# Optimization experiments

Measured on AMD Instinct MI355X. Metric: run time of the kernel, lower is better.

The kernel has to match this reference:

```python
import jax, jax.numpy as jnp
import numpy as np

NUM_CLASSES = 4
STRENGTH_INTER = 1.0
MOMENTUM = 0.99
EPS = 1e-8
LOG2 = 0.6931471805599453


def setup_inputs() -> dict:
    key = jax.random.key(0)
    k1, k2, k3, k4 = jax.random.split(key, 4)
    B, F, C, D, H, W = 2, 32, NUM_CLASSES, 64, 128, 128
    return {
        "features_to_modulate": jax.random.normal(k1, (B, F, D, H, W), dtype=jnp.float32),
        "logits_A": jax.random.normal(k2, (B, C, D, H, W), dtype=jnp.float32),
        "logits_B": jax.random.normal(k3, (B, C, D, H, W), dtype=jnp.float32),
        "pseudo_labels": jax.random.randint(k4, (B, D, H, W), 0, C, dtype=jnp.int64),
        "global_class_ranks": jnp.arange(C, dtype=jnp.float32),
    }


def _gamma_map(logits_A, logits_B, pseudo_labels, global_class_ranks):
    # JS-divergence disagreement map, summed over class channel (axis=1)
    logpA = jax.nn.log_softmax(logits_A, axis=1)
    logpB = jax.nn.log_softmax(logits_B, axis=1)
    pA = jnp.exp(logpA)
    pB = jnp.exp(logpB)
    logM = jnp.log(0.5 * (pA + pB) + EPS)
    kl_A = jnp.sum(pA * (logpA - logM), axis=1)  # [B,D,H,W]
    kl_B = jnp.sum(pB * (logpB - logM), axis=1)
    dis = 0.5 * (kl_A + kl_B)

    # per-class stats via segment reductions (single pass instead of per-class masking)
    lab_flat = pseudo_labels.reshape(-1)
    dis_flat = dis.reshape(-1)
    counts = jax.ops.segment_sum(jnp.ones_like(dis_flat), lab_flat, num_segments=NUM_CLASSES)
    seg_min = jax.ops.segment_min(dis_flat, lab_flat, num_segments=NUM_CLASSES)
    seg_max = jax.ops.segment_max(dis_flat, lab_flat, num_segments=NUM_CLASSES)
    present = counts > 0
    # EMA buffers start uninitialized (init: min=0, max=log 2); first call copies batch stats
    cls_min = jnp.where(present, seg_min, 0.0)
    cls_max = jnp.where(present, seg_max, LOG2)

    dmin = cls_min[pseudo_labels]
    dmax = cls_max[pseudo_labels]
    norm = jnp.where(dmax > dmin, (dis - dmin) / (dmax - dmin + EPS), 0.5)

    inter_term = 1.0 - global_class_ranks / (NUM_CLASSES - 1)
    inter_map = STRENGTH_INTER * inter_term[pseudo_labels]
    return 1.0 + inter_map * norm  # [B,D,H,W]


def reference(features_to_modulate, logits_A, logits_B, pseudo_labels, global_class_ranks):
    gamma_map = _gamma_map(logits_A, logits_B, pseudo_labels, global_class_ranks)
    scaled = features_to_modulate * gamma_map[:, None]  # broadcast over channel dim
    return scaled, gamma_map
```

## Files before the change

### kernel.cpp

```cpp
#include <hip/hip_runtime.h>
#include <hip/hip_bf16.h>

#define S_VOX  1048576
#define NVOX   2097152
#define NCLS   4
#define NFEAT  32
#define FEAT_ELEMS 67108864
#define EPS_F  1e-8f
#define LOG2_F 0.6931471805599453f
#define DIS_BLOCKS 1024

typedef float f32x4 __attribute__((ext_vector_type(4)));

__device__ __forceinline__ unsigned f2key(float f) {
    unsigned u = __float_as_uint(f);
    return (u & 0x80000000u) ? ~u : (u | 0x80000000u);
}
__device__ __forceinline__ float key2f(unsigned k) {
    unsigned u = (k & 0x80000000u) ? (k & 0x7FFFFFFFu) : ~k;
    return __uint_as_float(u);
}


__global__ void k_prolog(const unsigned* __restrict__ lab32, int* __restrict__ flag) {
    int t = threadIdx.x;
    unsigned even = lab32[2 * t];
    unsigned odd  = lab32[2 * t + 1];
    unsigned long long oddnz  = __ballot(odd  != 0u);
    unsigned long long evennz = __ballot(even != 0u);
    if (t == 0) *flag = (oddnz == 0ull && evennz != 0ull) ? 1 : 0;
}

__global__ void __launch_bounds__(256)
k_dis(const float* __restrict__ lA, const float* __restrict__ lB,
      const unsigned* __restrict__ lab32, const int* __restrict__ i64flag,
      float* __restrict__ dis, unsigned* __restrict__ partials) {
    __shared__ unsigned smin[NCLS], smax[NCLS];
    if (threadIdx.x < NCLS) { smin[threadIdx.x] = 0xFFFFFFFFu; smax[threadIdx.x] = 0u; }
    __syncthreads();

    const int lstride = 1 + *i64flag;
    unsigned lmin[NCLS] = {0xFFFFFFFFu, 0xFFFFFFFFu, 0xFFFFFFFFu, 0xFFFFFFFFu};
    unsigned lmax[NCLS] = {0u, 0u, 0u, 0u};

    const int nquad = NVOX / 4;
    for (int q = blockIdx.x * blockDim.x + threadIdx.x; q < nquad;
         q += gridDim.x * blockDim.x) {
        const int g = q << 2;
        const int b = g >> 20;
        const int v = g & (S_VOX - 1);
        const size_t abase = ((size_t)b * NCLS) * S_VOX + v;

        float4 a0 = *(const float4*)(lA + abase);
        float4 a1 = *(const float4*)(lA + abase + S_VOX);
        float4 a2 = *(const float4*)(lA + abase + 2 * (size_t)S_VOX);
        float4 a3 = *(const float4*)(lA + abase + 3 * (size_t)S_VOX);
        float4 c0 = *(const float4*)(lB + abase);
        float4 c1 = *(const float4*)(lB + abase + S_VOX);
        float4 c2 = *(const float4*)(lB + abase + 2 * (size_t)S_VOX);
        float4 c3 = *(const float4*)(lB + abase + 3 * (size_t)S_VOX);

        float dv[4];
        #pragma unroll
        for (int j = 0; j < 4; ++j) {
            float av[NCLS] = { ((const float*)&a0)[j], ((const float*)&a1)[j],
                               ((const float*)&a2)[j], ((const float*)&a3)[j] };
            float bv[NCLS] = { ((const float*)&c0)[j], ((const float*)&c1)[j],
                               ((const float*)&c2)[j], ((const float*)&c3)[j] };
            float maxA = fmaxf(fmaxf(av[0], av[1]), fmaxf(av[2], av[3]));
            float maxB = fmaxf(fmaxf(bv[0], bv[1]), fmaxf(bv[2], bv[3]));
            float eA[NCLS], eB[NCLS];
            float sA = 0.f, sB = 0.f;
            #pragma unroll
            for (int c = 0; c < NCLS; ++c) {
                eA[c] = __expf(av[c] - maxA); sA += eA[c];
                eB[c] = __expf(bv[c] - maxB); sB += eB[c];
            }
            float lseA = __logf(sA), lseB = __logf(sB);
            float rsA = 1.f / sA, rsB = 1.f / sB;
            float kl = 0.f;
            #pragma unroll
            for (int c = 0; c < NCLS; ++c) {
                float pA  = eA[c] * rsA;
                float pB  = eB[c] * rsB;
                float la  = av[c] - maxA - lseA;
                float lb  = bv[c] - maxB - lseB;
                float lM  = __logf(0.5f * (pA + pB) + EPS_F);
                kl += pA * (la - lM) + pB * (lb - lM);
            }
            dv[j] = 0.5f * kl;
        }

        *(float4*)(dis + g) = make_float4(dv[0], dv[1], dv[2], dv[3]);

        #pragma unroll
        for (int j = 0; j < 4; ++j) {
            int lbl = (int)lab32[(size_t)(g + j) * lstride];
            unsigned key = f2key(dv[j]);
            #pragma unroll
            for (int c = 0; c < NCLS; ++c) {
                if (lbl == c) {
                    lmin[c] = min(lmin[c], key);
                    lmax[c] = max(lmax[c], key);
                }
            }
        }
    }

    #pragma unroll
    for (int off = 32; off > 0; off >>= 1) {
        #pragma unroll
        for (int c = 0; c < NCLS; ++c) {
            unsigned om = (unsigned)__shfl_xor((int)lmin[c], off);
            unsigned oM = (unsigned)__shfl_xor((int)lmax[c], off);
            lmin[c] = min(lmin[c], om);
            lmax[c] = max(lmax[c], oM);
        }
    }
    if ((threadIdx.x & 63) == 0) {
        #pragma unroll
        for (int c = 0; c < NCLS; ++c) {
            atomicMin(&smin[c], lmin[c]);
            atomicMax(&smax[c], lmax[c]);
        }
    }
    __syncthreads();
    if (threadIdx.x < 8) {
        unsigned val = (threadIdx.x < NCLS) ? smin[threadIdx.x] : smax[threadIdx.x - NCLS];
        partials[(size_t)blockIdx.x * 8 + threadIdx.x] = val;
    }
}

__global__ void __launch_bounds__(256)
k_stats(const unsigned* __restrict__ partials, const float* __restrict__ ranks,
        float* __restrict__ params) {
    __shared__ unsigned red[4][8];
    const int tid = threadIdx.x;

    unsigned mn[NCLS] = {0xFFFFFFFFu, 0xFFFFFFFFu, 0xFFFFFFFFu, 0xFFFFFFFFu};
    unsigned mx[NCLS] = {0u, 0u, 0u, 0u};
    #pragma unroll
    for (int s = 0; s < 4; ++s) {
        const unsigned* p = partials + ((size_t)tid * 4 + s) * 8;
        uint4 pmin = *(const uint4*)(p);
        uint4 pmax = *(const uint4*)(p + 4);
        mn[0] = min(mn[0], pmin.x); mn[1] = min(mn[1], pmin.y);
        mn[2] = min(mn[2], pmin.z); mn[3] = min(mn[3], pmin.w);
        mx[0] = max(mx[0], pmax.x); mx[1] = max(mx[1], pmax.y);
        mx[2] = max(mx[2], pmax.z); mx[3] = max(mx[3], pmax.w);
    }
    #pragma unroll
    for (int off = 32; off > 0; off >>= 1) {
        #pragma unroll
        for (int c = 0; c < NCLS; ++c) {
            unsigned om = (unsigned)__shfl_xor((int)mn[c], off);
            unsigned oM = (unsigned)__shfl_xor((int)mx[c], off);
            mn[c] = min(mn[c], om);
            mx[c] = max(mx[c], oM);
        }
    }
    if ((tid & 63) == 0) {
        const int w = tid >> 6;
        #pragma unroll
        for (int c = 0; c < NCLS; ++c) { red[w][c] = mn[c]; red[w][NCLS + c] = mx[c]; }
    }
    __syncthreads();
    if (tid < NCLS) {
        const int c = tid;
        unsigned kmin = 0xFFFFFFFFu, kmax = 0u;
        #pragma unroll
        for (int w = 0; w < 4; ++w) {
            kmin = min(kmin, red[w][c]);
            kmax = max(kmax, red[w][NCLS + c]);
        }
        bool present = (kmin != 0xFFFFFFFFu);
        float dmin = present ? key2f(kmin) : 0.0f;
        float dmax = present ? key2f(kmax) : LOG2_F;
        float inter = 1.0f - ranks[c] * (1.0f / (NCLS - 1));
        float base, mult;
        if (dmax > dmin) {
            float inv = 1.0f / (dmax - dmin + EPS_F);
            mult = inter * inv;
            base = 1.0f - mult * dmin;
        } else {
            mult = 0.0f;
            base = 1.0f + 0.5f * inter;
        }
        params[c] = base;
        params[NCLS + c] = mult;
    }
}

__global__ void __launch_bounds__(256)
k_gamma(const unsigned* __restrict__ lab32, const int* __restrict__ i64flag,
        const float* __restrict__ dis, const float* __restrict__ params,
        float* __restrict__ gamma_out) {
    const int q = blockIdx.x * blockDim.x + threadIdx.x;
    const int g = q << 2;
    if (g >= NVOX) return;
    const int lstride = 1 + *i64flag;

    float4 d4 = *(const float4*)(dis + g);
    float ga[4];
    #pragma unroll
    for (int j = 0; j < 4; ++j) {
        int lbl = (int)lab32[(size_t)(g + j) * lstride];
        ga[j] = params[lbl] + params[NCLS + lbl] * ((const float*)&d4)[j];
    }
    *(float4*)(gamma_out + g) = make_float4(ga[0], ga[1], ga[2], ga[3]);
}

__global__ void __launch_bounds__(256)
k_scale(const float* __restrict__ feat, const float* __restrict__ gamma,
        float* __restrict__ out) {
    const size_t nchunk = FEAT_ELEMS / 4 / 512;
    for (size_t cb = blockIdx.x; cb < nchunk; cb += gridDim.x) {
        const size_t q0 = cb * 512 + threadIdx.x;
        const size_t e0 = q0 << 2;
        const size_t e1 = e0 + 1024;
        const size_t g0 = ((e0 >> 25) << 20) + (e0 & (size_t)(S_VOX - 1));
        const size_t g1 = ((e1 >> 25) << 20) + (e1 & (size_t)(S_VOX - 1));
        f32x4 x0 = __builtin_nontemporal_load((const f32x4*)(feat + e0));
        f32x4 x1 = __builtin_nontemporal_load((const f32x4*)(feat + e1));
        f32x4 m0 = *(const f32x4*)(gamma + g0);
        f32x4 m1 = *(const f32x4*)(gamma + g1);
        __builtin_nontemporal_store(x0 * m0, (f32x4*)(out + e0));
        __builtin_nontemporal_store(x1 * m1, (f32x4*)(out + e1));
    }
}

extern "C" void kernel_launch(void* const* d_in, const int* in_sizes, int n_in,
                              void* d_out, int out_size, void* d_ws, size_t ws_size,
                              hipStream_t stream) {
    const float*    feat  = (const float*)d_in[0];
    const float*    lA    = (const float*)d_in[1];
    const float*    lB    = (const float*)d_in[2];
    const unsigned* lab32 = (const unsigned*)d_in[3];
    const float*    ranks = (const float*)d_in[4];
    float* out = (float*)d_out;

    char* ws = (char*)d_ws;
    int*      flag     = (int*)(ws + 32);
    float*    params   = (float*)(ws + 64);
    float*    dis      = (float*)(ws + 256);
    unsigned* partials = (unsigned*)(ws + 256 + (size_t)NVOX * 4);

    float* gamma_out = out + (size_t)FEAT_ELEMS;

    k_prolog<<<1, 64, 0, stream>>>(lab32, flag);
    k_dis<<<DIS_BLOCKS, 256, 0, stream>>>(lA, lB, lab32, flag, dis, partials);
    k_stats<<<1, 256, 0, stream>>>(partials, ranks, params);
    k_gamma<<<NVOX / 4 / 256, 256, 0, stream>>>(lab32, flag, dis, params, gamma_out);
    k_scale<<<8192, 256, 0, stream>>>(feat, gamma_out, out);
}
```

Baseline: 130.7 us.

## Fuse gamma computation into scale kernel using label-packed dis values

Packs the 2-bit pseudo label into the low mantissa bits of each disagreement value, so one 32-bit word carries both. The separate gamma kernel is removed: the scale kernel rebuilds gamma from the packed word and the per-class params, multiplies the features, and the feature-0 blocks also write the gamma output. This drops one launch and the extra read and write pass over dis, labels and gamma. In exchange the two low mantissa bits of dis are dropped (a small precision loss), and gamma is recomputed once for each of the 32 feature channels.

```diff
diff --git a/kernel.cpp b/kernel.cpp
--- a/kernel.cpp
+++ b/kernel.cpp
@@ -34,7 +34,7 @@
 __global__ void __launch_bounds__(256)
 k_dis(const float* __restrict__ lA, const float* __restrict__ lB,
       const unsigned* __restrict__ lab32, const int* __restrict__ i64flag,
-      float* __restrict__ dis, unsigned* __restrict__ partials) {
+      unsigned* __restrict__ disp, unsigned* __restrict__ partials) {
     __shared__ unsigned smin[NCLS], smax[NCLS];
     if (threadIdx.x < NCLS) { smin[threadIdx.x] = 0xFFFFFFFFu; smax[threadIdx.x] = 0u; }
     __syncthreads();
@@ -91,15 +91,23 @@
             dv[j] = 0.5f * kl;
         }
 
-        *(float4*)(dis + g) = make_float4(dv[0], dv[1], dv[2], dv[3]);
+        unsigned lbls[4];
+        #pragma unroll
+        for (int j = 0; j < 4; ++j)
+            lbls[j] = lab32[(size_t)(g + j) * lstride] & 3u;
+
+        unsigned pw[4];
+        #pragma unroll
+        for (int j = 0; j < 4; ++j)
+            pw[j] = (__float_as_uint(dv[j]) & ~3u) | lbls[j];
+        *(uint4*)(disp + g) = make_uint4(pw[0], pw[1], pw[2], pw[3]);
 
         #pragma unroll
         for (int j = 0; j < 4; ++j) {
-            int lbl = (int)lab32[(size_t)(g + j) * lstride];
             unsigned key = f2key(dv[j]);
             #pragma unroll
             for (int c = 0; c < NCLS; ++c) {
-                if (lbl == c) {
+                if (lbls[j] == (unsigned)c) {
                     lmin[c] = min(lmin[c], key);
                     lmax[c] = max(lmax[c], key);
                 }
@@ -192,40 +200,51 @@
 }
 
 __global__ void __launch_bounds__(256)
-k_gamma(const unsigned* __restrict__ lab32, const int* __restrict__ i64flag,
-        const float* __restrict__ dis, const float* __restrict__ params,
-        float* __restrict__ gamma_out) {
-    const int q = blockIdx.x * blockDim.x + threadIdx.x;
-    const int g = q << 2;
-    if (g >= NVOX) return;
-    const int lstride = 1 + *i64flag;
-
-    float4 d4 = *(const float4*)(dis + g);
-    float ga[4];
-    #pragma unroll
-    for (int j = 0; j < 4; ++j) {
-        int lbl = (int)lab32[(size_t)(g + j) * lstride];
-        ga[j] = params[lbl] + params[NCLS + lbl] * ((const float*)&d4)[j];
-    }
-    *(float4*)(gamma_out + g) = make_float4(ga[0], ga[1], ga[2], ga[3]);
-}
-
-__global__ void __launch_bounds__(256)
-k_scale(const float* __restrict__ feat, const float* __restrict__ gamma,
+k_scale(const float* __restrict__ feat, const unsigned* __restrict__ disp,
+        const float* __restrict__ params, float* __restrict__ gamma_out,
         float* __restrict__ out) {
-    const size_t nchunk = FEAT_ELEMS / 4 / 512;
+    const float b0 = params[0], b1 = params[1], b2 = params[2], b3 = params[3];
+    const float m0 = params[4], m1 = params[5], m2 = params[6], m3 = params[7];
+
+    const size_t nchunk = FEAT_ELEMS / 4096;
     for (size_t cb = blockIdx.x; cb < nchunk; cb += gridDim.x) {
-        const size_t q0 = cb * 512 + threadIdx.x;
-        const size_t e0 = q0 << 2;
-        const size_t e1 = e0 + 1024;
-        const size_t g0 = ((e0 >> 25) << 20) + (e0 & (size_t)(S_VOX - 1));
-        const size_t g1 = ((e1 >> 25) << 20) + (e1 & (size_t)(S_VOX - 1));
+        const int f0 = (int)((cb >> 8) & 31);
+        const size_t e0 = (cb << 12) + ((size_t)threadIdx.x << 2);
+        const size_t gb = ((cb >> 13) << 20) + ((cb << 12) & (size_t)(S_VOX - 1))
+                          + ((size_t)threadIdx.x << 2);
+
         f32x4 x0 = __builtin_nontemporal_load((const f32x4*)(feat + e0));
-        f32x4 x1 = __builtin_nontemporal_load((const f32x4*)(feat + e1));
-        f32x4 m0 = *(const f32x4*)(gamma + g0);
-        f32x4 m1 = *(const f32x4*)(gamma + g1);
-        __builtin_nontemporal_store(x0 * m0, (f32x4*)(out + e0));
-        __builtin_nontemporal_store(x1 * m1, (f32x4*)(out + e1));
+        f32x4 x1 = __builtin_nontemporal_load((const f32x4*)(feat + e0 + 1024));
+        f32x4 x2 = __builtin_nontemporal_load((const f32x4*)(feat + e0 + 2048));
+        f32x4 x3 = __builtin_nontemporal_load((const f32x4*)(feat + e0 + 3072));
+
+        f32x4 ga[4];
+        #pragma unroll
+        for (int u = 0; u < 4; ++u) {
+            uint4 dp = *(const uint4*)(disp + gb + (size_t)u * 1024);
+            const unsigned dw[4] = { dp.x, dp.y, dp.z, dp.w };
+            #pragma unroll
+            for (int j = 0; j < 4; ++j) {
+                const unsigned lbl = dw[j] & 3u;
+                const float d = __uint_as_float(dw[j]);
+                const float bb = (lbl & 1u) ? ((lbl & 2u) ? b3 : b1)
+                                            : ((lbl & 2u) ? b2 : b0);
+                const float mm = (lbl & 1u) ? ((lbl & 2u) ? m3 : m1)
+                                            : ((lbl & 2u) ? m2 : m0);
+                ga[u][j] = fmaf(mm, d, bb);
+            }
+        }
+
+        __builtin_nontemporal_store(x0 * ga[0], (f32x4*)(out + e0));
+        __builtin_nontemporal_store(x1 * ga[1], (f32x4*)(out + e0 + 1024));
+        __builtin_nontemporal_store(x2 * ga[2], (f32x4*)(out + e0 + 2048));
+        __builtin_nontemporal_store(x3 * ga[3], (f32x4*)(out + e0 + 3072));
+
+        if (f0 == 0) {
+            #pragma unroll
+            for (int u = 0; u < 4; ++u)
+                *(f32x4*)(gamma_out + gb + (size_t)u * 1024) = ga[u];
+        }
     }
 }
 
@@ -242,14 +261,13 @@
     char* ws = (char*)d_ws;
     int*      flag     = (int*)(ws + 32);
     float*    params   = (float*)(ws + 64);
-    float*    dis      = (float*)(ws + 256);
+    unsigned* disp     = (unsigned*)(ws + 256);
     unsigned* partials = (unsigned*)(ws + 256 + (size_t)NVOX * 4);
 
     float* gamma_out = out + (size_t)FEAT_ELEMS;
 
     k_prolog<<<1, 64, 0, stream>>>(lab32, flag);
-    k_dis<<<DIS_BLOCKS, 256, 0, stream>>>(lA, lB, lab32, flag, dis, partials);
+    k_dis<<<DIS_BLOCKS, 256, 0, stream>>>(lA, lB, lab32, flag, disp, partials);
     k_stats<<<1, 256, 0, stream>>>(partials, ranks, params);
-    k_gamma<<<NVOX / 4 / 256, 256, 0, stream>>>(lab32, flag, dis, params, gamma_out);
-    k_scale<<<8192, 256, 0, stream>>>(feat, gamma_out, out);
-}
+    k_scale<<<8192, 256, 0, stream>>>(feat, disp, params, gamma_out, out);
+}
```

Result: faster. 124.6 us (-4.7%).
